# Optimization experiments

Hardware: AMD Instinct MI355X
Metric: run time of the kernel (lower is better)

Reference implementation:

```python
import jax, jax.numpy as jnp
import numpy as np

N_NODES = 10000
N_EDGES = 160000
B = 128
HEADS = 4
DIMS = [36, 128, 256, 512]
NEG_SLOPE = 0.2  # PyG GATConv default


def setup_inputs() -> dict:
    key = jax.random.key(0)
    ks = jax.random.split(key, 32)
    inp = {}
    inp["x"] = jax.random.normal(ks[0], (N_NODES, DIMS[0]), jnp.float32)
    inp["edge_index"] = jax.random.randint(ks[1], (2, N_EDGES), 0, N_NODES)
    inp["batch"] = jnp.sort(jax.random.randint(ks[2], (N_NODES,), 0, B))
    ki = 3
    for i in range(3):
        din, dout = DIMS[i], DIMS[i + 1]
        C = dout // HEADS
        inp[f"gcn_w{i}"] = jax.random.normal(ks[ki], (din, dout), jnp.float32) * (din ** -0.5); ki += 1
        inp[f"gcn_b{i}"] = jnp.zeros((dout,), jnp.float32)
        inp[f"gat_w{i}"] = jax.random.normal(ks[ki], (dout, dout), jnp.float32) * (dout ** -0.5); ki += 1
        inp[f"gat_as{i}"] = jax.random.normal(ks[ki], (HEADS, C), jnp.float32) * 0.1; ki += 1
        inp[f"gat_ad{i}"] = jax.random.normal(ks[ki], (HEADS, C), jnp.float32) * 0.1; ki += 1
        inp[f"gat_b{i}"] = jnp.zeros((dout,), jnp.float32)
    D = DIMS[-1]
    inp["ap_w1"] = jax.random.normal(ks[ki], (D, D // 2), jnp.float32) * (D ** -0.5); ki += 1
    inp["ap_b1"] = jnp.zeros((D // 2,), jnp.float32)
    inp["ap_w2"] = jax.random.normal(ks[ki], (D // 2, 1), jnp.float32) * ((D // 2) ** -0.5); ki += 1
    inp["ap_b2"] = jnp.zeros((1,), jnp.float32)
    return inp


def _gcn(x, w, b, src, dst, n):
    # PyG GCNConv: add self-loops, symmetric deg^-1/2 normalization, bias after agg
    h = x @ w  # [N, dout]
    deg = jax.ops.segment_sum(jnp.ones_like(dst, dtype=h.dtype), dst, n) + 1.0  # incl. self-loop
    dinv = deg ** -0.5
    norm = dinv[src] * dinv[dst]  # [E]
    agg = jax.ops.segment_sum(h[src] * norm[:, None], dst, n)
    agg = agg + h * (dinv * dinv)[:, None]  # self-loop messages
    return agg + b


def _gat(x, w, a_s, a_d, b, src, dst, n):
    # PyG GATConv: self-loops, leaky-relu logits, segment softmax over dst, concat heads
    C = w.shape[1] // HEADS
    h = (x @ w).reshape(n, HEADS, C)
    alpha_src = (h * a_s).sum(-1)  # [N, H]
    alpha_dst = (h * a_d).sum(-1)  # [N, H]
    loop = jnp.arange(n)
    s = jnp.concatenate([src, loop])
    d = jnp.concatenate([dst, loop])
    e = jax.nn.leaky_relu(alpha_src[s] + alpha_dst[d], NEG_SLOPE)  # [E+N, H]
    m = jax.ops.segment_max(e, d, n)
    ex = jnp.exp(e - m[d])
    den = jax.ops.segment_sum(ex, d, n)
    alpha = ex / den[d]  # [E+N, H]
    out = jax.ops.segment_sum(h[s] * alpha[:, :, None], d, n)  # [N, H, C]
    return out.reshape(n, HEADS * C) + b


def _forward(x, edge_index, batch, params, ap_w1, ap_b1, ap_w2, ap_b2):
    src, dst = edge_index[0], edge_index[1]
    n = x.shape[0]
    x_in = x
    n_layers = len(params)
    for i, (gw, gb, aw, a_s, a_d, ab) in enumerate(params):
        h = jax.nn.relu(_gcn(x, gw, gb, src, dst, n))  # dropout is identity in eval
        x = h + _gat(h, aw, a_s, a_d, ab, src, dst, n)
        if i < n_layers - 1:
            if x.shape[-1] == x_in.shape[-1]:
                x = x + x_in
            x_in = x
    # attention pooling (global softmax then per-graph masked renorm)
    a = jnp.tanh(x @ ap_w1 + ap_b1) @ ap_w2 + ap_b2  # [N, 1]
    a = jax.nn.softmax(a, axis=0)
    mask = jax.nn.one_hot(batch, B, dtype=x.dtype)  # [N, B]
    aw_ = a * mask
    aw_ = aw_ / (aw_.sum(0, keepdims=True) + 1e-8)
    graph_emb = aw_.T @ x  # [B, D]
    cnt = jax.ops.segment_sum(jnp.ones((n,), x.dtype), batch, B)
    ssum = jax.ops.segment_sum(x, batch, B)
    mean = ssum / jnp.maximum(cnt, 1.0)[:, None]
    smax = jax.ops.segment_max(x, batch, B)
    return jnp.concatenate([graph_emb, mean, smax, ssum], axis=1)  # [B, 4*D]


def reference(x, edge_index, batch,
              gcn_w0, gcn_b0, gat_w0, gat_as0, gat_ad0, gat_b0,
              gcn_w1, gcn_b1, gat_w1, gat_as1, gat_ad1, gat_b1,
              gcn_w2, gcn_b2, gat_w2, gat_as2, gat_ad2, gat_b2,
              ap_w1, ap_b1, ap_w2, ap_b2):
    params = [
        (gcn_w0, gcn_b0, gat_w0, gat_as0, gat_ad0, gat_b0),
        (gcn_w1, gcn_b1, gat_w1, gat_as1, gat_ad1, gat_b1),
        (gcn_w2, gcn_b2, gat_w2, gat_as2, gat_ad2, gat_b2),
    ]
    return _forward(x, edge_index, batch, params, ap_w1, ap_b1, ap_w2, ap_b2)
```

## Files before the change

### kernel.cpp

```cpp
#include <hip/hip_runtime.h>
#include <math.h>

#define NN 10000
#define NE 160000
#define NB 128
#define NH 4
#define DOUT 512
#define NEG 0.2f
#define SCAN_BLKS ((NN + 255) / 256)
#define CNT_BLKS ((NE + 255) / 256)

typedef __attribute__((ext_vector_type(8))) short short8;
typedef __attribute__((ext_vector_type(4))) float f32x4;
typedef __attribute__((ext_vector_type(4))) unsigned short us4;

__device__ __forceinline__ float leakyf(float v){ return v > 0.f ? v : NEG*v; }
__device__ __forceinline__ void fma4(float4& a, const float4 v, float w){
  a.x += v.x*w; a.y += v.y*w; a.z += v.z*w; a.w += v.w*w;
}
__device__ __forceinline__ void mul4(float4& a, float s){
  a.x *= s; a.y *= s; a.z *= s; a.w *= s;
}
__device__ __forceinline__ unsigned short f2bf(float f){
  unsigned int u = __float_as_uint(f);
  u += 0x7FFFu + ((u >> 16) & 1u);
  return (unsigned short)(u >> 16);
}
__device__ __forceinline__ float bf2f(unsigned short h){
  return __uint_as_float(((unsigned int)h) << 16);
}
__device__ __forceinline__ void split2(float v, unsigned short& h, unsigned short& l){
  h = f2bf(v);
  l = f2bf(v - bf2f(h));
}
__device__ __forceinline__ void store_hl(unsigned short* H, unsigned short* L,
                                         size_t base, float4 v){
  us4 h, l; unsigned short hh, ll;
  split2(v.x, hh, ll); h[0]=hh; l[0]=ll;
  split2(v.y, hh, ll); h[1]=hh; l[1]=ll;
  split2(v.z, hh, ll); h[2]=hh; l[2]=ll;
  split2(v.w, hh, ll); h[3]=hh; l[3]=ll;
  *(us4*)&H[base] = h;
  *(us4*)&L[base] = l;
}
__device__ __forceinline__ float4 load_hl(const unsigned short* __restrict__ H,
                                          const unsigned short* __restrict__ L, size_t base){
  us4 h = *(const us4*)&H[base];
  us4 l = *(const us4*)&L[base];
  return make_float4(bf2f(h[0])+bf2f(l[0]), bf2f(h[1])+bf2f(l[1]),
                     bf2f(h[2])+bf2f(l[2]), bf2f(h[3])+bf2f(l[3]));
}
__device__ __forceinline__ void gl_lds16(const unsigned short* g, unsigned short* l){
  __builtin_amdgcn_global_load_lds(
      (const __attribute__((address_space(1))) unsigned int*)g,
      (__attribute__((address_space(3))) unsigned int*)l, 16, 0, 0);
}

struct AllConv {
  const float* src[7];
  unsigned short* dh[7];
  unsigned short* dl[7];
  int K[7], Mm[7], Kp[7], tot[7];
};

__global__ void k_count_conv(const int* __restrict__ dst, int* __restrict__ cnt,
                             AllConv a, int convTot){
  int bid = blockIdx.x;
  if (bid < CNT_BLKS){
    int e = bid*256 + threadIdx.x;
    if (e < NE) atomicAdd(&cnt[dst[e]], 1);
  } else {
    int idx = (bid - CNT_BLKS)*256 + threadIdx.x;
    if (idx >= convTot) return;
    int j = 0;
    while (idx >= a.tot[j]){ idx -= a.tot[j]; j++; }
    int Kp = a.Kp[j], K = a.K[j], M = a.Mm[j];
    int kk = idx % Kp, m = idx / Kp;
    float v = (kk < K) ? a.src[j][(size_t)kk*M + m] : 0.f;
    unsigned short h, l; split2(v, h, l);
    a.dh[j][idx] = h; a.dl[j][idx] = l;
  }
}
__global__ void k_scan1(const int* __restrict__ cnt, int* __restrict__ bsum,
                        const int* __restrict__ batch, int* __restrict__ starts){
  __shared__ int red[256];
  int blk = blockIdx.x, t = threadIdx.x;
  int idx = blk*256 + t;
  red[t] = (idx < NN) ? cnt[idx] : 0;
  __syncthreads();
  for (int o = 128; o > 0; o >>= 1){
    if (t < o) red[t] += red[t + o];
    __syncthreads();
  }
  if (t == 0) bsum[blk] = red[0];
  if (blk == 0 && t <= NB){
    int lo = 0, hi = NN;
    while (lo < hi){ int mid = (lo + hi) >> 1; if (batch[mid] < t) lo = mid + 1; else hi = mid; }
    starts[t] = lo;
  }
}
__global__ void k_scan3(const int* __restrict__ cnt, const int* __restrict__ bsum,
                        int* __restrict__ rowptr, float* __restrict__ dinv,
                        int* __restrict__ cursor, float* __restrict__ apre){
  __shared__ int s[256];
  __shared__ int base_s;
  int blk = blockIdx.x, t = threadIdx.x;
  int idx = blk*256 + t;
  int c = (idx < NN) ? cnt[idx] : 0;
  s[t] = c;
  if (t == 0){
    int acc = 0;
    for (int i = 0; i < blk; i++) acc += bsum[i];
    base_s = acc;
    if (blk == SCAN_BLKS - 1){
      int tot = acc;
      for (int i = blk; i < SCAN_BLKS; i++) tot += bsum[i];
      rowptr[NN] = tot;
    }
  }
  __syncthreads();
  for (int o = 1; o < 256; o <<= 1){
    int v = 0;
    if (t >= o) v = s[t - o];
    __syncthreads();
    if (t >= o) s[t] += v;
    __syncthreads();
  }
  if (idx < NN){
    rowptr[idx] = base_s + s[t] - c;
    dinv[idx] = rsqrtf((float)c + 1.f);
    cursor[idx] = 0;
    apre[idx] = 0.f;
  }
}
__global__ void k_fill(const int* __restrict__ src, const int* __restrict__ dst,
                       const int* __restrict__ rowptr, int* __restrict__ cursor,
                       int* __restrict__ colidx){
  int e = blockIdx.x*blockDim.x + threadIdx.x;
  if (e >= NE) return;
  int d = dst[e];
  int pos = atomicAdd(&cursor[d], 1);
  colidx[rowptr[d] + pos] = src[e];
}

#define GBM 64
#define GBN 128
#define GBK 32
__global__ __launch_bounds__(256) void k_gemm_bf3(
    const unsigned short* __restrict__ Ah, const unsigned short* __restrict__ Al,
    const unsigned short* __restrict__ Bh, const unsigned short* __restrict__ Bl,
    float* __restrict__ C, int N, int Kp, int M, int mode,
    const float* __restrict__ bias, unsigned short* __restrict__ outH,
    unsigned short* __restrict__ outL,
    const float* __restrict__ a_s, const float* __restrict__ a_d,
    float* __restrict__ as_o, float* __restrict__ ad_o, int Cdim){
  __shared__ unsigned short AsH[GBM*GBK], AsL[GBM*GBK];
  __shared__ unsigned short BsH[GBN*GBK], BsL[GBN*GBK];
  __shared__ float sred[2][GBM][4];
  int gx = M / GBN;
  int gy = (N + GBM - 1) / GBM;
  const int G = 8;
  int bid = blockIdx.x;
  int full = gy / G;
  int bid_full = full * G * gx;
  int by, bx;
  if (bid < bid_full){
    int g = bid / (G*gx); int rem = bid % (G*gx);
    by = g*G + rem % G; bx = rem / G;
  } else {
    int rem = bid - bid_full; int rows = gy - full*G;
    by = full*G + rem % rows; bx = rem / rows;
  }
  int row0 = by * GBM, col0 = bx * GBN;
  int t = threadIdx.x;
  int w = t >> 6, L = t & 63;
  int lm = L & 15, lq = L >> 4;
  int wc = w * 32;

  int sr = L >> 2, sc = L & 3;
  int art = w*16 + sr;
  int ga  = (sc - ((art >> 1) & 3)) & 3;
  int agrow = min(row0 + art, N-1);
  int brt0 = w*16 + sr;
  int brt1 = (w+4)*16 + sr;
  int gb0 = (sc - ((brt0 >> 1) & 3)) & 3;
  int gb1 = (sc - ((brt1 >> 1) & 3)) & 3;
  int bgrow0 = col0 + brt0, bgrow1 = col0 + brt1;

  int rc = (lq + (lm >> 1)) & 3;
  int aoff[4], boff[2];
#pragma unroll
  for (int mi = 0; mi < 4; mi++) aoff[mi] = (mi*16 + lm)*32 + rc*8;
#pragma unroll
  for (int ni = 0; ni < 2; ni++) boff[ni] = (wc + ni*16 + lm)*32 + rc*8;

  f32x4 acc[4][2];
#pragma unroll
  for (int i = 0; i < 4; i++)
#pragma unroll
    for (int j = 0; j < 2; j++) acc[i][j] = (f32x4){0.f,0.f,0.f,0.f};

  int nk = Kp / GBK;
  for (int kt = 0; kt < nk; kt++){
    int k0 = kt * GBK;
    if (kt) __syncthreads();
    gl_lds16(&Ah[(size_t)agrow*Kp + k0 + ga*8],  &AsH[w*512]);
    gl_lds16(&Al[(size_t)agrow*Kp + k0 + ga*8],  &AsL[w*512]);
    gl_lds16(&Bh[(size_t)bgrow0*Kp + k0 + gb0*8], &BsH[w*512]);
    gl_lds16(&Bh[(size_t)bgrow1*Kp + k0 + gb1*8], &BsH[(w+4)*512]);
    gl_lds16(&Bl[(size_t)bgrow0*Kp + k0 + gb0*8], &BsL[w*512]);
    gl_lds16(&Bl[(size_t)bgrow1*Kp + k0 + gb1*8], &BsL[(w+4)*512]);
    __syncthreads();

    short8 ah[4], al[4], bh[2], bl[2];
#pragma unroll
    for (int mi = 0; mi < 4; mi++){
      ah[mi] = *(const short8*)&AsH[aoff[mi]];
      al[mi] = *(const short8*)&AsL[aoff[mi]];
    }
#pragma unroll
    for (int ni = 0; ni < 2; ni++){
      bh[ni] = *(const short8*)&BsH[boff[ni]];
      bl[ni] = *(const short8*)&BsL[boff[ni]];
    }
#pragma unroll
    for (int mi = 0; mi < 4; mi++)
#pragma unroll
      for (int ni = 0; ni < 2; ni++){
        acc[mi][ni] = __builtin_amdgcn_mfma_f32_16x16x32_bf16(ah[mi], bh[ni], acc[mi][ni], 0, 0, 0);
        acc[mi][ni] = __builtin_amdgcn_mfma_f32_16x16x32_bf16(ah[mi], bl[ni], acc[mi][ni], 0, 0, 0);
        acc[mi][ni] = __builtin_amdgcn_mfma_f32_16x16x32_bf16(al[mi], bh[ni], acc[mi][ni], 0, 0, 0);
      }
  }
  if (mode == 1){
#pragma unroll
    for (int mi = 0; mi < 4; mi++)
#pragma unroll
      for (int ni = 0; ni < 2; ni++){
#pragma unroll
        for (int r = 0; r < 4; r++){
          int row = row0 + mi*16 + lq*4 + r;
          int col = col0 + wc + ni*16 + lm;
          if (row < N){
            float v = fmaxf(acc[mi][ni][r] + bias[col], 0.f);
            unsigned short hh, ll; split2(v, hh, ll);
            outH[(size_t)row*M + col] = hh;
            outL[(size_t)row*M + col] = ll;
          }
        }
      }
  } else if (mode != 3){
#pragma unroll
    for (int mi = 0; mi < 4; mi++)
#pragma unroll
      for (int ni = 0; ni < 2; ni++){
#pragma unroll
        for (int r = 0; r < 4; r++){
          int row = row0 + mi*16 + lq*4 + r;
          int col = col0 + wc + ni*16 + lm;
          if (row < N) C[(size_t)row*M + col] = acc[mi][ni][r];
        }
      }
  }
  if (mode == 2){
    float sA0 = a_s[col0 + wc + lm], sA1 = a_s[col0 + wc + 16 + lm];
    float dA0 = a_d[col0 + wc + lm], dA1 = a_d[col0 + wc + 16 + lm];
#pragma unroll
    for (int mi = 0; mi < 4; mi++)
#pragma unroll
      for (int r = 0; r < 4; r++){
        float vs = acc[mi][0][r]*sA0 + acc[mi][1][r]*sA1;
        float vd = acc[mi][0][r]*dA0 + acc[mi][1][r]*dA1;
#pragma unroll
        for (int o = 1; o <= 8; o <<= 1){
          vs += __shfl_xor(vs, o);
          vd += __shfl_xor(vd, o);
        }
        if (lm == 0){
          int row = mi*16 + lq*4 + r;
          sred[0][row][w] = vs;
          sred[1][row][w] = vd;
        }
      }
    __syncthreads();
    if (t < GBM){
      int n = row0 + t;
      if (n < N){
        int wph = Cdim >> 5;
        int nheads = 4 / wph;
        for (int g = 0; g < nheads; g++){
          float ss = 0.f, dd = 0.f;
          for (int q = 0; q < wph; q++){
            ss += sred[0][t][g*wph + q];
            dd += sred[1][t][g*wph + q];
          }
          int hd = (col0 + g*wph*32) / Cdim;
          as_o[n*NH + hd] = ss;
          ad_o[n*NH + hd] = dd;
        }
      }
    }
  } else if (mode == 3){
    float b0 = bias[col0 + wc + lm], b1v = bias[col0 + wc + 16 + lm];
    float w0v = a_s[col0 + wc + lm], w1v = a_s[col0 + wc + 16 + lm];
#pragma unroll
    for (int mi = 0; mi < 4; mi++)
#pragma unroll
      for (int r = 0; r < 4; r++){
        float v = tanhf(acc[mi][0][r] + b0)*w0v + tanhf(acc[mi][1][r] + b1v)*w1v;
#pragma unroll
        for (int o = 1; o <= 8; o <<= 1) v += __shfl_xor(v, o);
        if (lm == 0) sred[0][mi*16 + lq*4 + r][w] = v;
      }
    __syncthreads();
    if (t < GBM){
      int n = row0 + t;
      if (n < N){
        float s = sred[0][t][0] + sred[0][t][1] + sred[0][t][2] + sred[0][t][3];
        atomicAdd(&as_o[n], s);
      }
    }
  }
}

__global__ __launch_bounds__(256) void k_gcn_pre0(
    const float* __restrict__ x0, const float* __restrict__ dinv,
    const int* __restrict__ rowptr, const int* __restrict__ colidx,
    unsigned short* __restrict__ outH, unsigned short* __restrict__ outL){
  int t = threadIdx.x;
  int sub = t & 15;
  int n = blockIdx.x*16 + (t >> 4);
  if (n >= NN) return;
  int f0 = sub*4;
  bool act = f0 < 36;
  int b = rowptr[n], e = rowptr[n+1];
  float dn = dinv[n];
  float4 a0 = make_float4(0,0,0,0), a1 = make_float4(0,0,0,0);
  float4 a2 = make_float4(0,0,0,0), a3 = make_float4(0,0,0,0);
  if (act){
    int j = b;
    for (; j + 3 < e; j += 4){
      int s0 = colidx[j], s1 = colidx[j+1], s2 = colidx[j+2], s3 = colidx[j+3];
      float w0 = dinv[s0], w1 = dinv[s1], w2 = dinv[s2], w3 = dinv[s3];
      float4 v0 = *(const float4*)&x0[(size_t)s0*36 + f0];
      float4 v1 = *(const float4*)&x0[(size_t)s1*36 + f0];
      float4 v2 = *(const float4*)&x0[(size_t)s2*36 + f0];
      float4 v3 = *(const float4*)&x0[(size_t)s3*36 + f0];
      fma4(a0, v0, w0*dn); fma4(a1, v1, w1*dn);
      fma4(a2, v2, w2*dn); fma4(a3, v3, w3*dn);
    }
    for (; j < e; j++){
      int s = colidx[j];
      float4 v = *(const float4*)&x0[(size_t)s*36 + f0];
      fma4(a0, v, dinv[s]*dn);
    }
  }
  float4 acc = make_float4(a0.x+a1.x+a2.x+a3.x, a0.y+a1.y+a2.y+a3.y,
                           a0.z+a1.z+a2.z+a3.z, a0.w+a1.w+a2.w+a3.w);
  if (act){
    float4 sv = *(const float4*)&x0[(size_t)n*36 + f0];
    float dn2 = dn*dn;
    acc.x += sv.x*dn2; acc.y += sv.y*dn2; acc.z += sv.z*dn2; acc.w += sv.w*dn2;
  }
  store_hl(outH, outL, (size_t)n*64 + f0, acc);
}

__global__ __launch_bounds__(256) void k_gcn_pre(
    const unsigned short* __restrict__ inH, const unsigned short* __restrict__ inL,
    const float* __restrict__ dinv,
    const int* __restrict__ rowptr, const int* __restrict__ colidx,
    unsigned short* __restrict__ outH, unsigned short* __restrict__ outL,
    int Kp, int nchunk){
  int bid = blockIdx.x;
  int chunk = bid % nchunk, grp = bid / nchunk;
  int t = threadIdx.x;
  int sub = t & 15;
  int n = grp*16 + (t >> 4);
  if (n >= NN) return;
  int f0 = chunk*64 + sub*4;
  int b = rowptr[n], e = rowptr[n+1];
  float dn = dinv[n];
  float4 a0 = make_float4(0,0,0,0), a1 = make_float4(0,0,0,0);
  float4 a2 = make_float4(0,0,0,0), a3 = make_float4(0,0,0,0);
  int j = b;
  for (; j + 3 < e; j += 4){
    int s0 = colidx[j], s1 = colidx[j+1], s2 = colidx[j+2], s3 = colidx[j+3];
    float w0 = dinv[s0], w1 = dinv[s1], w2 = dinv[s2], w3 = dinv[s3];
    float4 v0 = load_hl(inH, inL, (size_t)s0*Kp + f0);
    float4 v1 = load_hl(inH, inL, (size_t)s1*Kp + f0);
    float4 v2 = load_hl(inH, inL, (size_t)s2*Kp + f0);
    float4 v3 = load_hl(inH, inL, (size_t)s3*Kp + f0);
    fma4(a0, v0, w0*dn); fma4(a1, v1, w1*dn);
    fma4(a2, v2, w2*dn); fma4(a3, v3, w3*dn);
  }
  for (; j < e; j++){
    int s = colidx[j];
    float4 v = load_hl(inH, inL, (size_t)s*Kp + f0);
    fma4(a0, v, dinv[s]*dn);
  }
  float4 acc = make_float4(a0.x+a1.x+a2.x+a3.x, a0.y+a1.y+a2.y+a3.y,
                           a0.z+a1.z+a2.z+a3.z, a0.w+a1.w+a2.w+a3.w);
  float4 sv = load_hl(inH, inL, (size_t)n*Kp + f0);
  float dn2 = dn*dn;
  acc.x += sv.x*dn2; acc.y += sv.y*dn2; acc.z += sv.z*dn2; acc.w += sv.w*dn2;
  store_hl(outH, outL, (size_t)n*Kp + f0, acc);
}

__global__ __launch_bounds__(256) void k_gat_gather(
    const float* __restrict__ hg,
    const unsigned short* __restrict__ inH, const unsigned short* __restrict__ inL,
    const int* __restrict__ rowptr, const int* __restrict__ colidx,
    const float* __restrict__ as_, const float* __restrict__ ad_,
    const float* __restrict__ ab,
    unsigned short* __restrict__ outH, unsigned short* __restrict__ outL,
    int M, int C, int nchunk){
  int bid = blockIdx.x;
  int chunk = bid % nchunk, grp = bid / nchunk;
  int t = threadIdx.x;
  int sub = t & 15;
  int n = grp*16 + (t >> 4);
  if (n >= NN) return;
  int f0 = chunk*64 + sub*4;
  int hd = f0 / C;
  int b = rowptr[n], e = rowptr[n+1];
  int ai = n*NH + hd;
  float adn = ad_[ai];
  float selflog = leakyf(as_[ai] + adn);
  float m = selflog, d = 1.f;
  float4 a0 = make_float4(0,0,0,0), a1 = make_float4(0,0,0,0);
  float4 a2 = make_float4(0,0,0,0), a3 = make_float4(0,0,0,0);
  int j = b;
  for (; j + 3 < e; j += 4){
    int s0 = colidx[j], s1 = colidx[j+1], s2 = colidx[j+2], s3 = colidx[j+3];
    float l0 = leakyf(as_[s0*NH + hd] + adn), l1 = leakyf(as_[s1*NH + hd] + adn);
    float l2 = leakyf(as_[s2*NH + hd] + adn), l3 = leakyf(as_[s3*NH + hd] + adn);
    float4 v0 = *(const float4*)&hg[(size_t)s0*M + f0];
    float4 v1 = *(const float4*)&hg[(size_t)s1*M + f0];
    float4 v2 = *(const float4*)&hg[(size_t)s2*M + f0];
    float4 v3 = *(const float4*)&hg[(size_t)s3*M + f0];
    float m4 = fmaxf(fmaxf(l0, l1), fmaxf(l2, l3));
    if (m4 > m){
      float sc = expf(m - m4);
      d *= sc; mul4(a0, sc); mul4(a1, sc); mul4(a2, sc); mul4(a3, sc);
      m = m4;
    }
    float w0 = expf(l0 - m), w1 = expf(l1 - m);
    float w2 = expf(l2 - m), w3 = expf(l3 - m);
    d += (w0 + w1) + (w2 + w3);
    fma4(a0, v0, w0); fma4(a1, v1, w1);
    fma4(a2, v2, w2); fma4(a3, v3, w3);
  }
  for (; j < e; j++){
    int s = colidx[j];
    float l = leakyf(as_[s*NH + hd] + adn);
    float4 v = *(const float4*)&hg[(size_t)s*M + f0];
    if (l > m){
      float sc = expf(m - l);
      d *= sc; mul4(a0, sc); mul4(a1, sc); mul4(a2, sc); mul4(a3, sc);
      m = l;
    }
    float ww = expf(l - m);
    d += ww;
    fma4(a0, v, ww);
  }
  float4 acc = make_float4(a0.x+a1.x+a2.x+a3.x, a0.y+a1.y+a2.y+a3.y,
                           a0.z+a1.z+a2.z+a3.z, a0.w+a1.w+a2.w+a3.w);
  float es = expf(selflog - m), inv = 1.f/d;
  float4 sv = *(const float4*)&hg[(size_t)n*M + f0];
  float4 hv = load_hl(inH, inL, (size_t)n*M + f0);
  float4 bb = *(const float4*)&ab[f0];
  float4 r = make_float4(
    hv.x + bb.x + (sv.x*es + acc.x)*inv,
    hv.y + bb.y + (sv.y*es + acc.y)*inv,
    hv.z + bb.z + (sv.z*es + acc.z)*inv,
    hv.w + bb.w + (sv.w*es + acc.w)*inv);
  store_hl(outH, outL, (size_t)n*M + f0, r);
}

__global__ void k_pool(const unsigned short* __restrict__ xH, const unsigned short* __restrict__ xL,
                       const float* __restrict__ apre, const int* __restrict__ starts,
                       float* __restrict__ out){
  __shared__ float red[128];
  int g = blockIdx.x, t = threadIdx.x;
  int b = starts[g], e = starts[g+1];
  float m = -INFINITY;
  for (int n = b + t; n < e; n += 128) m = fmaxf(m, apre[n]);
  red[t] = m; __syncthreads();
  for (int o = 64; o > 0; o >>= 1){
    if (t < o) red[t] = fmaxf(red[t], red[t + o]);
    __syncthreads();
  }
  m = red[0]; __syncthreads();
  float s = 0.f;
  for (int n = b + t; n < e; n += 128) s += expf(apre[n] - m);
  red[t] = s; __syncthreads();
  for (int o = 64; o > 0; o >>= 1){
    if (t < o) red[t] += red[t + o];
    __syncthreads();
  }
  float inv = 1.f / (red[0] + 1e-8f);
  float4 sum = make_float4(0,0,0,0), wacc = make_float4(0,0,0,0);
  float4 mx = make_float4(-INFINITY,-INFINITY,-INFINITY,-INFINITY);
  for (int n = b; n < e; n++){
    float4 xv = load_hl(xH, xL, (size_t)n*DOUT + t*4);
    float p = expf(apre[n] - m) * inv;
    sum.x += xv.x; sum.y += xv.y; sum.z += xv.z; sum.w += xv.w;
    mx.x = fmaxf(mx.x, xv.x); mx.y = fmaxf(mx.y, xv.y);
    mx.z = fmaxf(mx.z, xv.z); mx.w = fmaxf(mx.w, xv.w);
    fma4(wacc, xv, p);
  }
  float ic = 1.f / fmaxf((float)(e - b), 1.f);
  float4* o = (float4*)(out + (size_t)g*4*DOUT);
  o[t]       = wacc;
  o[128 + t] = make_float4(sum.x*ic, sum.y*ic, sum.z*ic, sum.w*ic);
  o[256 + t] = mx;
  o[384 + t] = sum;
}

extern "C" void kernel_launch(void* const* d_in, const int* in_sizes, int n_in,
                              void* d_out, int out_size, void* d_ws, size_t ws_size,
                              hipStream_t stream) {
  const float* x0   = (const float*)d_in[0];
  const int*   ei   = (const int*)d_in[1];
  const int*   src  = ei;
  const int*   dst  = ei + NE;
  const int*   batch= (const int*)d_in[2];
  const float* gw[3]  = {(const float*)d_in[3],  (const float*)d_in[9],  (const float*)d_in[15]};
  const float* gb[3]  = {(const float*)d_in[4],  (const float*)d_in[10], (const float*)d_in[16]};
  const float* aw[3]  = {(const float*)d_in[5],  (const float*)d_in[11], (const float*)d_in[17]};
  const float* asw[3] = {(const float*)d_in[6],  (const float*)d_in[12], (const float*)d_in[18]};
  const float* adw[3] = {(const float*)d_in[7],  (const float*)d_in[13], (const float*)d_in[19]};
  const float* ab[3]  = {(const float*)d_in[8],  (const float*)d_in[14], (const float*)d_in[20]};
  const float* apw1 = (const float*)d_in[21];
  const float* apb1 = (const float*)d_in[22];
  const float* apw2 = (const float*)d_in[23];
  float* out = (float*)d_out;

  char* p = (char*)d_ws;
  auto alloc = [&](size_t bytes) -> void* {
    void* r = (void*)p; p += (bytes + 255) & ~(size_t)255; return r;
  };
  float* f1 = (float*)alloc((size_t)NN*512*4);
  unsigned short* actH0 = (unsigned short*)alloc((size_t)NN*512*2);
  unsigned short* actL0 = (unsigned short*)alloc((size_t)NN*512*2);
  unsigned short* actH1 = (unsigned short*)alloc((size_t)NN*512*2);
  unsigned short* actL1 = (unsigned short*)alloc((size_t)NN*512*2);
  unsigned short* preH  = (unsigned short*)alloc((size_t)NN*256*2);
  unsigned short* preL  = (unsigned short*)alloc((size_t)NN*256*2);
  const int wK[7]  = {36, 128, 128, 256, 256, 512, 512};
  const int wM[7]  = {128, 128, 256, 256, 512, 512, 256};
  const int wKp[7] = {64, 128, 128, 256, 256, 512, 512};
  const float* wsrc[7] = {gw[0], aw[0], gw[1], aw[1], gw[2], aw[2], apw1};
  unsigned short* wTh[7]; unsigned short* wTl[7];
  for (int i = 0; i < 7; i++){
    size_t sz = (size_t)wM[i]*wKp[i]*2;
    wTh[i] = (unsigned short*)alloc(sz);
    wTl[i] = (unsigned short*)alloc(sz);
  }
  float* dinv = (float*)alloc(NN*4);
  float* as_  = (float*)alloc(NN*NH*4);
  float* ad_  = (float*)alloc(NN*NH*4);
  float* apre = (float*)alloc(NN*4);
  int* rowptr = (int*)alloc((NN+1)*4);
  int* colidx = (int*)alloc((size_t)NE*4);
  int* cnt    = (int*)alloc(NN*4);
  int* cursor = (int*)alloc(NN*4);
  int* starts = (int*)alloc((NB+1)*4);
  int* bsum   = (int*)alloc(SCAN_BLKS*4);

  AllConv ac;
  int convTot = 0;
  for (int i = 0; i < 7; i++){
    ac.src[i] = wsrc[i]; ac.dh[i] = wTh[i]; ac.dl[i] = wTl[i];
    ac.K[i] = wK[i]; ac.Mm[i] = wM[i]; ac.Kp[i] = wKp[i];
    ac.tot[i] = wKp[i]*wM[i];
    convTot += ac.tot[i];
  }

  hipMemsetAsync(cnt, 0, NN*sizeof(int), stream);
  int convBlks = (convTot + 255) / 256;
  k_count_conv<<<CNT_BLKS + convBlks, 256, 0, stream>>>(dst, cnt, ac, convTot);
  k_scan1<<<SCAN_BLKS, 256, 0, stream>>>(cnt, bsum, batch, starts);
  k_scan3<<<SCAN_BLKS, 256, 0, stream>>>(cnt, bsum, rowptr, dinv, cursor, apre);
  k_fill<<<(NE+255)/256, 256, 0, stream>>>(src, dst, rowptr, cursor, colidx);

  const int dims[4] = {36, 128, 256, 512};
  const int ngrp = (NN + 15) / 16;
  const unsigned short* curH = nullptr; const unsigned short* curL = nullptr;
  int wi = 0;
  for (int i = 0; i < 3; i++){
    int Kin = (i == 0) ? 64 : dims[i];
    int M = dims[i+1], C = M/NH;
    int nchunk_in = Kin / 64;
    int nchunk = M / 64;
    int nblk = (M/GBN) * ((NN+GBM-1)/GBM);
    if (i == 0){
      k_gcn_pre0<<<ngrp, 256, 0, stream>>>(x0, dinv, rowptr, colidx, preH, preL);
    } else {
      k_gcn_pre<<<nchunk_in*ngrp, 256, 0, stream>>>(curH, curL, dinv, rowptr, colidx,
                                                    preH, preL, Kin, nchunk_in);
    }
    k_gemm_bf3<<<nblk, 256, 0, stream>>>(preH, preL, wTh[wi], wTl[wi], f1, NN, wKp[wi], M,
                                         1, gb[i], actH0, actL0,
                                         nullptr, nullptr, nullptr, nullptr, C);
    wi++;
    k_gemm_bf3<<<nblk, 256, 0, stream>>>(actH0, actL0, wTh[wi], wTl[wi], f1, NN, wKp[wi], M,
                                         2, nullptr, nullptr, nullptr,
                                         asw[i], adw[i], as_, ad_, C);
    wi++;
    k_gat_gather<<<nchunk*ngrp, 256, 0, stream>>>(f1, actH0, actL0, rowptr, colidx,
                                                  as_, ad_, ab[i],
                                                  actH1, actL1, M, C, nchunk);
    curH = actH1; curL = actL1;
  }

  {
    int nblk = (256/GBN) * ((NN+GBM-1)/GBM);
    k_gemm_bf3<<<nblk, 256, 0, stream>>>(actH1, actL1, wTh[6], wTl[6], f1, NN, wKp[6], 256,
                                         3, apb1, nullptr, nullptr,
                                         apw2, nullptr, apre, nullptr, 64);
  }
  k_pool<<<NB, 128, 0, stream>>>(actH1, actL1, apre, starts, out);
}
```

Measured before the change: 397.8 us.

## Merge scan kernels, unroll gathers by eight, and parallelize pooling across node slices

Replaces the two-kernel block scan with a single 1024-thread kernel that stages the counts in shared memory, saving one launch and the serial bsum loop. The CSR gather loops in the GCN and GAT kernels gain an 8-wide unrolled path and hoist the self-node loads so more memory requests are in flight at once. The pooling kernel moves to 512 threads, with four node slices combined through shared memory, which gives more parallelism per graph. Costs are a single-block scan that relies on 40KB of shared memory, and higher register pressure from the wider unrolls.

```diff
diff --git a/kernel.cpp b/kernel.cpp
--- a/kernel.cpp
+++ b/kernel.cpp
@@ -7,7 +7,6 @@
 #define NH 4
 #define DOUT 512
 #define NEG 0.2f
-#define SCAN_BLKS ((NN + 255) / 256)
 #define CNT_BLKS ((NE + 255) / 256)
 
 typedef __attribute__((ext_vector_type(8))) short short8;
@@ -81,58 +80,49 @@
     a.dh[j][idx] = h; a.dl[j][idx] = l;
   }
 }
-__global__ void k_scan1(const int* __restrict__ cnt, int* __restrict__ bsum,
-                        const int* __restrict__ batch, int* __restrict__ starts){
-  __shared__ int red[256];
-  int blk = blockIdx.x, t = threadIdx.x;
-  int idx = blk*256 + t;
-  red[t] = (idx < NN) ? cnt[idx] : 0;
-  __syncthreads();
-  for (int o = 128; o > 0; o >>= 1){
-    if (t < o) red[t] += red[t + o];
-    __syncthreads();
-  }
-  if (t == 0) bsum[blk] = red[0];
-  if (blk == 0 && t <= NB){
+
+__global__ __launch_bounds__(1024) void k_scan_all(
+    const int* __restrict__ cnt, const int* __restrict__ batch,
+    int* __restrict__ rowptr, float* __restrict__ dinv,
+    int* __restrict__ cursor, float* __restrict__ apre,
+    int* __restrict__ starts){
+  __shared__ int sh[NN];
+  __shared__ int pref[1024];
+  int t = threadIdx.x;
+  for (int i = t; i < NN; i += 1024) sh[i] = cnt[i];
+  if (t <= NB){
     int lo = 0, hi = NN;
     while (lo < hi){ int mid = (lo + hi) >> 1; if (batch[mid] < t) lo = mid + 1; else hi = mid; }
     starts[t] = lo;
   }
-}
-__global__ void k_scan3(const int* __restrict__ cnt, const int* __restrict__ bsum,
-                        int* __restrict__ rowptr, float* __restrict__ dinv,
-                        int* __restrict__ cursor, float* __restrict__ apre){
-  __shared__ int s[256];
-  __shared__ int base_s;
-  int blk = blockIdx.x, t = threadIdx.x;
-  int idx = blk*256 + t;
-  int c = (idx < NN) ? cnt[idx] : 0;
-  s[t] = c;
-  if (t == 0){
-    int acc = 0;
-    for (int i = 0; i < blk; i++) acc += bsum[i];
-    base_s = acc;
-    if (blk == SCAN_BLKS - 1){
-      int tot = acc;
-      for (int i = blk; i < SCAN_BLKS; i++) tot += bsum[i];
-      rowptr[NN] = tot;
-    }
-  }
   __syncthreads();
-  for (int o = 1; o < 256; o <<= 1){
-    int v = 0;
-    if (t >= o) v = s[t - o];
+  int base = t*10;
+  int csum = 0;
+#pragma unroll
+  for (int k = 0; k < 10; k++){ int i = base + k; if (i < NN) csum += sh[i]; }
+  pref[t] = csum; __syncthreads();
+  for (int o = 1; o < 1024; o <<= 1){
+    int v = (t >= o) ? pref[t - o] : 0;
     __syncthreads();
-    if (t >= o) s[t] += v;
+    pref[t] += v;
     __syncthreads();
   }
-  if (idx < NN){
-    rowptr[idx] = base_s + s[t] - c;
-    dinv[idx] = rsqrtf((float)c + 1.f);
-    cursor[idx] = 0;
-    apre[idx] = 0.f;
-  }
-}
+  int run = pref[t] - csum;
+#pragma unroll
+  for (int k = 0; k < 10; k++){
+    int i = base + k;
+    if (i < NN){
+      int c = sh[i];
+      rowptr[i] = run;
+      run += c;
+      dinv[i] = rsqrtf((float)c + 1.f);
+      cursor[i] = 0;
+      apre[i] = 0.f;
+    }
+  }
+  if (t == 1023) rowptr[NN] = pref[1023];
+}
+
 __global__ void k_fill(const int* __restrict__ src, const int* __restrict__ dst,
                        const int* __restrict__ rowptr, int* __restrict__ cursor,
                        int* __restrict__ colidx){
@@ -338,7 +328,26 @@
   float4 a0 = make_float4(0,0,0,0), a1 = make_float4(0,0,0,0);
   float4 a2 = make_float4(0,0,0,0), a3 = make_float4(0,0,0,0);
   if (act){
+    float4 sv = *(const float4*)&x0[(size_t)n*36 + f0];
     int j = b;
+    for (; j + 7 < e; j += 8){
+      int s0 = colidx[j],   s1 = colidx[j+1], s2 = colidx[j+2], s3 = colidx[j+3];
+      int s4 = colidx[j+4], s5 = colidx[j+5], s6 = colidx[j+6], s7 = colidx[j+7];
+      float w0 = dinv[s0], w1 = dinv[s1], w2 = dinv[s2], w3 = dinv[s3];
+      float w4 = dinv[s4], w5 = dinv[s5], w6 = dinv[s6], w7 = dinv[s7];
+      float4 v0 = *(const float4*)&x0[(size_t)s0*36 + f0];
+      float4 v1 = *(const float4*)&x0[(size_t)s1*36 + f0];
+      float4 v2 = *(const float4*)&x0[(size_t)s2*36 + f0];
+      float4 v3 = *(const float4*)&x0[(size_t)s3*36 + f0];
+      float4 v4 = *(const float4*)&x0[(size_t)s4*36 + f0];
+      float4 v5 = *(const float4*)&x0[(size_t)s5*36 + f0];
+      float4 v6 = *(const float4*)&x0[(size_t)s6*36 + f0];
+      float4 v7 = *(const float4*)&x0[(size_t)s7*36 + f0];
+      fma4(a0, v0, w0*dn); fma4(a1, v1, w1*dn);
+      fma4(a2, v2, w2*dn); fma4(a3, v3, w3*dn);
+      fma4(a0, v4, w4*dn); fma4(a1, v5, w5*dn);
+      fma4(a2, v6, w6*dn); fma4(a3, v7, w7*dn);
+    }
     for (; j + 3 < e; j += 4){
       int s0 = colidx[j], s1 = colidx[j+1], s2 = colidx[j+2], s3 = colidx[j+3];
       float w0 = dinv[s0], w1 = dinv[s1], w2 = dinv[s2], w3 = dinv[s3];
@@ -354,15 +363,14 @@
       float4 v = *(const float4*)&x0[(size_t)s*36 + f0];
       fma4(a0, v, dinv[s]*dn);
     }
-  }
-  float4 acc = make_float4(a0.x+a1.x+a2.x+a3.x, a0.y+a1.y+a2.y+a3.y,
-                           a0.z+a1.z+a2.z+a3.z, a0.w+a1.w+a2.w+a3.w);
-  if (act){
-    float4 sv = *(const float4*)&x0[(size_t)n*36 + f0];
+    float4 acc = make_float4(a0.x+a1.x+a2.x+a3.x, a0.y+a1.y+a2.y+a3.y,
+                             a0.z+a1.z+a2.z+a3.z, a0.w+a1.w+a2.w+a3.w);
     float dn2 = dn*dn;
     acc.x += sv.x*dn2; acc.y += sv.y*dn2; acc.z += sv.z*dn2; acc.w += sv.w*dn2;
-  }
-  store_hl(outH, outL, (size_t)n*64 + f0, acc);
+    store_hl(outH, outL, (size_t)n*64 + f0, acc);
+  } else {
+    store_hl(outH, outL, (size_t)n*64 + f0, make_float4(0,0,0,0));
+  }
 }
 
 __global__ __launch_bounds__(256) void k_gcn_pre(
@@ -380,9 +388,28 @@
   int f0 = chunk*64 + sub*4;
   int b = rowptr[n], e = rowptr[n+1];
   float dn = dinv[n];
+  float4 sv = load_hl(inH, inL, (size_t)n*Kp + f0);
   float4 a0 = make_float4(0,0,0,0), a1 = make_float4(0,0,0,0);
   float4 a2 = make_float4(0,0,0,0), a3 = make_float4(0,0,0,0);
   int j = b;
+  for (; j + 7 < e; j += 8){
+    int s0 = colidx[j],   s1 = colidx[j+1], s2 = colidx[j+2], s3 = colidx[j+3];
+    int s4 = colidx[j+4], s5 = colidx[j+5], s6 = colidx[j+6], s7 = colidx[j+7];
+    float w0 = dinv[s0], w1 = dinv[s1], w2 = dinv[s2], w3 = dinv[s3];
+    float w4 = dinv[s4], w5 = dinv[s5], w6 = dinv[s6], w7 = dinv[s7];
+    float4 v0 = load_hl(inH, inL, (size_t)s0*Kp + f0);
+    float4 v1 = load_hl(inH, inL, (size_t)s1*Kp + f0);
+    float4 v2 = load_hl(inH, inL, (size_t)s2*Kp + f0);
+    float4 v3 = load_hl(inH, inL, (size_t)s3*Kp + f0);
+    float4 v4 = load_hl(inH, inL, (size_t)s4*Kp + f0);
+    float4 v5 = load_hl(inH, inL, (size_t)s5*Kp + f0);
+    float4 v6 = load_hl(inH, inL, (size_t)s6*Kp + f0);
+    float4 v7 = load_hl(inH, inL, (size_t)s7*Kp + f0);
+    fma4(a0, v0, w0*dn); fma4(a1, v1, w1*dn);
+    fma4(a2, v2, w2*dn); fma4(a3, v3, w3*dn);
+    fma4(a0, v4, w4*dn); fma4(a1, v5, w5*dn);
+    fma4(a2, v6, w6*dn); fma4(a3, v7, w7*dn);
+  }
   for (; j + 3 < e; j += 4){
     int s0 = colidx[j], s1 = colidx[j+1], s2 = colidx[j+2], s3 = colidx[j+3];
     float w0 = dinv[s0], w1 = dinv[s1], w2 = dinv[s2], w3 = dinv[s3];
@@ -400,7 +427,6 @@
   }
   float4 acc = make_float4(a0.x+a1.x+a2.x+a3.x, a0.y+a1.y+a2.y+a3.y,
                            a0.z+a1.z+a2.z+a3.z, a0.w+a1.w+a2.w+a3.w);
-  float4 sv = load_hl(inH, inL, (size_t)n*Kp + f0);
   float dn2 = dn*dn;
   acc.x += sv.x*dn2; acc.y += sv.y*dn2; acc.z += sv.z*dn2; acc.w += sv.w*dn2;
   store_hl(outH, outL, (size_t)n*Kp + f0, acc);
@@ -426,10 +452,45 @@
   int ai = n*NH + hd;
   float adn = ad_[ai];
   float selflog = leakyf(as_[ai] + adn);
+  float4 sv = *(const float4*)&hg[(size_t)n*M + f0];
+  float4 hv = load_hl(inH, inL, (size_t)n*M + f0);
+  float4 bb = *(const float4*)&ab[f0];
   float m = selflog, d = 1.f;
   float4 a0 = make_float4(0,0,0,0), a1 = make_float4(0,0,0,0);
   float4 a2 = make_float4(0,0,0,0), a3 = make_float4(0,0,0,0);
   int j = b;
+  for (; j + 7 < e; j += 8){
+    int s0 = colidx[j],   s1 = colidx[j+1], s2 = colidx[j+2], s3 = colidx[j+3];
+    int s4 = colidx[j+4], s5 = colidx[j+5], s6 = colidx[j+6], s7 = colidx[j+7];
+    float l0 = leakyf(as_[s0*NH + hd] + adn), l1 = leakyf(as_[s1*NH + hd] + adn);
+    float l2 = leakyf(as_[s2*NH + hd] + adn), l3 = leakyf(as_[s3*NH + hd] + adn);
+    float l4 = leakyf(as_[s4*NH + hd] + adn), l5 = leakyf(as_[s5*NH + hd] + adn);
+    float l6 = leakyf(as_[s6*NH + hd] + adn), l7 = leakyf(as_[s7*NH + hd] + adn);
+    float4 v0 = *(const float4*)&hg[(size_t)s0*M + f0];
+    float4 v1 = *(const float4*)&hg[(size_t)s1*M + f0];
+    float4 v2 = *(const float4*)&hg[(size_t)s2*M + f0];
+    float4 v3 = *(const float4*)&hg[(size_t)s3*M + f0];
+    float4 v4 = *(const float4*)&hg[(size_t)s4*M + f0];
+    float4 v5 = *(const float4*)&hg[(size_t)s5*M + f0];
+    float4 v6 = *(const float4*)&hg[(size_t)s6*M + f0];
+    float4 v7 = *(const float4*)&hg[(size_t)s7*M + f0];
+    float m8 = fmaxf(fmaxf(fmaxf(l0, l1), fmaxf(l2, l3)),
+                     fmaxf(fmaxf(l4, l5), fmaxf(l6, l7)));
+    if (m8 > m){
+      float sc = expf(m - m8);
+      d *= sc; mul4(a0, sc); mul4(a1, sc); mul4(a2, sc); mul4(a3, sc);
+      m = m8;
+    }
+    float w0 = expf(l0 - m), w1 = expf(l1 - m);
+    float w2 = expf(l2 - m), w3 = expf(l3 - m);
+    float w4 = expf(l4 - m), w5 = expf(l5 - m);
+    float w6 = expf(l6 - m), w7 = expf(l7 - m);
+    d += ((w0 + w1) + (w2 + w3)) + ((w4 + w5) + (w6 + w7));
+    fma4(a0, v0, w0); fma4(a1, v1, w1);
+    fma4(a2, v2, w2); fma4(a3, v3, w3);
+    fma4(a0, v4, w4); fma4(a1, v5, w5);
+    fma4(a2, v6, w6); fma4(a3, v7, w7);
+  }
   for (; j + 3 < e; j += 4){
     int s0 = colidx[j], s1 = colidx[j+1], s2 = colidx[j+2], s3 = colidx[j+3];
     float l0 = leakyf(as_[s0*NH + hd] + adn), l1 = leakyf(as_[s1*NH + hd] + adn);
@@ -466,9 +527,6 @@
   float4 acc = make_float4(a0.x+a1.x+a2.x+a3.x, a0.y+a1.y+a2.y+a3.y,
                            a0.z+a1.z+a2.z+a3.z, a0.w+a1.w+a2.w+a3.w);
   float es = expf(selflog - m), inv = 1.f/d;
-  float4 sv = *(const float4*)&hg[(size_t)n*M + f0];
-  float4 hv = load_hl(inH, inL, (size_t)n*M + f0);
-  float4 bb = *(const float4*)&ab[f0];
   float4 r = make_float4(
     hv.x + bb.x + (sv.x*es + acc.x)*inv,
     hv.y + bb.y + (sv.y*es + acc.y)*inv,
@@ -477,44 +535,59 @@
   store_hl(outH, outL, (size_t)n*M + f0, r);
 }
 
-__global__ void k_pool(const unsigned short* __restrict__ xH, const unsigned short* __restrict__ xL,
-                       const float* __restrict__ apre, const int* __restrict__ starts,
-                       float* __restrict__ out){
-  __shared__ float red[128];
+__global__ __launch_bounds__(512) void k_pool(
+    const unsigned short* __restrict__ xH, const unsigned short* __restrict__ xL,
+    const float* __restrict__ apre, const int* __restrict__ starts,
+    float* __restrict__ out){
+  __shared__ float red[512];
+  __shared__ float4 comb[3][4][128];
   int g = blockIdx.x, t = threadIdx.x;
   int b = starts[g], e = starts[g+1];
   float m = -INFINITY;
-  for (int n = b + t; n < e; n += 128) m = fmaxf(m, apre[n]);
+  for (int n = b + t; n < e; n += 512) m = fmaxf(m, apre[n]);
   red[t] = m; __syncthreads();
-  for (int o = 64; o > 0; o >>= 1){
+  for (int o = 256; o > 0; o >>= 1){
     if (t < o) red[t] = fmaxf(red[t], red[t + o]);
     __syncthreads();
   }
   m = red[0]; __syncthreads();
   float s = 0.f;
-  for (int n = b + t; n < e; n += 128) s += expf(apre[n] - m);
+  for (int n = b + t; n < e; n += 512) s += expf(apre[n] - m);
   red[t] = s; __syncthreads();
-  for (int o = 64; o > 0; o >>= 1){
+  for (int o = 256; o > 0; o >>= 1){
     if (t < o) red[t] += red[t + o];
     __syncthreads();
   }
   float inv = 1.f / (red[0] + 1e-8f);
+  int lf = t & 127, sl = t >> 7;
   float4 sum = make_float4(0,0,0,0), wacc = make_float4(0,0,0,0);
   float4 mx = make_float4(-INFINITY,-INFINITY,-INFINITY,-INFINITY);
-  for (int n = b; n < e; n++){
-    float4 xv = load_hl(xH, xL, (size_t)n*DOUT + t*4);
+  for (int n = b + sl; n < e; n += 4){
+    float4 xv = load_hl(xH, xL, (size_t)n*DOUT + lf*4);
     float p = expf(apre[n] - m) * inv;
     sum.x += xv.x; sum.y += xv.y; sum.z += xv.z; sum.w += xv.w;
     mx.x = fmaxf(mx.x, xv.x); mx.y = fmaxf(mx.y, xv.y);
     mx.z = fmaxf(mx.z, xv.z); mx.w = fmaxf(mx.w, xv.w);
     fma4(wacc, xv, p);
   }
-  float ic = 1.f / fmaxf((float)(e - b), 1.f);
-  float4* o = (float4*)(out + (size_t)g*4*DOUT);
-  o[t]       = wacc;
-  o[128 + t] = make_float4(sum.x*ic, sum.y*ic, sum.z*ic, sum.w*ic);
-  o[256 + t] = mx;
-  o[384 + t] = sum;
+  comb[0][sl][lf] = wacc; comb[1][sl][lf] = sum; comb[2][sl][lf] = mx;
+  __syncthreads();
+  if (sl == 0){
+#pragma unroll
+    for (int q = 1; q < 4; q++){
+      float4 w2 = comb[0][q][lf], s2 = comb[1][q][lf], m2 = comb[2][q][lf];
+      wacc.x += w2.x; wacc.y += w2.y; wacc.z += w2.z; wacc.w += w2.w;
+      sum.x += s2.x; sum.y += s2.y; sum.z += s2.z; sum.w += s2.w;
+      mx.x = fmaxf(mx.x, m2.x); mx.y = fmaxf(mx.y, m2.y);
+      mx.z = fmaxf(mx.z, m2.z); mx.w = fmaxf(mx.w, m2.w);
+    }
+    float ic = 1.f / fmaxf((float)(e - b), 1.f);
+    float4* o = (float4*)(out + (size_t)g*4*DOUT);
+    o[lf]       = wacc;
+    o[128 + lf] = make_float4(sum.x*ic, sum.y*ic, sum.z*ic, sum.w*ic);
+    o[256 + lf] = mx;
+    o[384 + lf] = sum;
+  }
 }
 
 extern "C" void kernel_launch(void* const* d_in, const int* in_sizes, int n_in,
@@ -566,7 +639,6 @@
   int* cnt    = (int*)alloc(NN*4);
   int* cursor = (int*)alloc(NN*4);
   int* starts = (int*)alloc((NB+1)*4);
-  int* bsum   = (int*)alloc(SCAN_BLKS*4);
 
   AllConv ac;
   int convTot = 0;
@@ -580,8 +652,7 @@
   hipMemsetAsync(cnt, 0, NN*sizeof(int), stream);
   int convBlks = (convTot + 255) / 256;
   k_count_conv<<<CNT_BLKS + convBlks, 256, 0, stream>>>(dst, cnt, ac, convTot);
-  k_scan1<<<SCAN_BLKS, 256, 0, stream>>>(cnt, bsum, batch, starts);
-  k_scan3<<<SCAN_BLKS, 256, 0, stream>>>(cnt, bsum, rowptr, dinv, cursor, apre);
+  k_scan_all<<<1, 1024, 0, stream>>>(cnt, batch, rowptr, dinv, cursor, apre, starts);
   k_fill<<<(NE+255)/256, 256, 0, stream>>>(src, dst, rowptr, cursor, colidx);
 
   const int dims[4] = {36, 128, 256, 512};
@@ -620,5 +691,5 @@
                                          3, apb1, nullptr, nullptr,
                                          apw2, nullptr, apre, nullptr, 64);
   }
-  k_pool<<<NB, 128, 0, stream>>>(actH1, actL1, apre, starts, out);
-}
+  k_pool<<<NB, 512, 0, stream>>>(actH1, actL1, apre, starts, out);
+}
```

New measurement: 393.1 us. Within noise of the previous version (-1.2%).
